# Kernel optimization log

Measured on AMD Instinct MI355X. Metric: run time of the kernel, lower is better.

Reference implementation:

```python
import jax, jax.numpy as jnp
import numpy as np

N, M, D = 1024, 32, 512
EPS = 1e-6


def setup_inputs() -> dict:
    key = jax.random.key(0)
    k1, = jax.random.split(key, 1)
    dvecs = jax.random.normal(k1, (N, M, D), dtype=jnp.float32)
    w = jnp.float32(10.0)
    b = jnp.float32(-5.0)
    return {"dvecs": dvecs, "w": w, "b": b}


def reference(dvecs, w, b):
    # dvecs: (N, M, D)
    n, m, d = dvecs.shape
    centroids = dvecs.mean(axis=1)                     # (N, D) full centroids
    # leave-one-out centroid for the reference utterance's own speaker
    c_loo = (dvecs.sum(axis=1, keepdims=True) - dvecs) / (m - 1)   # (N, M, D)

    e_norm = jnp.linalg.norm(dvecs, axis=-1)           # (N, M)
    c_norm = jnp.linalg.norm(centroids, axis=-1)       # (N,)
    c_loo_norm = jnp.linalg.norm(c_loo, axis=-1)       # (N, M)

    # cosine sim against all full centroids: (N, M, N)
    cos = jnp.einsum('jmd,kd->jmk', dvecs, centroids) / (
        e_norm[:, :, None] * c_norm[None, None, :])
    # replace the own-speaker entry with leave-one-out cosine
    loo_cos = jnp.einsum('jmd,jmd->jm', dvecs, c_loo) / (e_norm * c_loo_norm)
    jidx = jnp.arange(n)
    midx = jnp.arange(m)
    cos = cos.at[jidx[:, None], midx[None, :], jidx[:, None]].set(loo_cos)

    # torch.clamp(x, 1e-6) clamps the minimum only
    cos = jnp.maximum(cos, EPS) * w + b

    # softmax embed loss: L[j,i] = -log_softmax(cos[j,i,:])[j]
    logp = jax.nn.log_softmax(cos, axis=-1)
    L = -logp[jidx[:, None], midx[None, :], jidx[:, None]]
    return L.sum()
```

## Files before the change

kernel.cpp:

```cpp
#include <hip/hip_runtime.h>
#include <hip/hip_bf16.h>

#define NSPK 1024
#define MU 32
#define DIM 512
#define DIMP (DIM + 8)
#define NROW (NSPK * MU)
#define EPS 1e-6f

typedef __attribute__((ext_vector_type(4))) float f32x4;
typedef __attribute__((ext_vector_type(2))) long i64x2;

#define GLOAD_LDS16(g, l)                                          \
  __builtin_amdgcn_global_load_lds(                                \
      (const __attribute__((address_space(1))) void*)(g),          \
      (__attribute__((address_space(3))) void*)(l), 16, 0, 0)

__global__ __launch_bounds__(256) void k_prep(
    const float* __restrict__ dvecs,
    char* __restrict__ Af8,
    char* __restrict__ Bf8,
    float* __restrict__ loo)
{
  const int j = blockIdx.x, t = threadIdx.x;
  __shared__ float sD[MU * DIMP];
  __shared__ float4 sHalf[2][128];
  __shared__ float sS[DIM];
  __shared__ float sred[4];
  __shared__ float sS2v;
  __shared__ float sInv[MU];

  const float* base = dvecs + (size_t)j * (MU * DIM);

  const int h = t >> 7, c4 = t & 127;
  {
    const float* bp = base + h * 16 * DIM + c4 * 4;
    float4 cs = make_float4(0.f, 0.f, 0.f, 0.f);
#pragma unroll
    for (int m = 0; m < 16; ++m) {
      float4 v = *(const float4*)(bp + m * DIM);
      *(float4*)&sD[(h * 16 + m) * DIMP + c4 * 4] = v;
      cs.x += v.x; cs.y += v.y; cs.z += v.z; cs.w += v.w;
    }
    sHalf[h][c4] = cs;
  }
  __syncthreads();
  if (t < 128) {
    float4 a = sHalf[0][t], b2 = sHalf[1][t];
    float4 s;
    s.x = a.x + b2.x; s.y = a.y + b2.y; s.z = a.z + b2.z; s.w = a.w + b2.w;
    *(float4*)&sS[t * 4] = s;
  }
  __syncthreads();

  float p = sS[t] * sS[t] + sS[t + 256] * sS[t + 256];
  for (int off = 32; off; off >>= 1) p += __shfl_down(p, off);
  if ((t & 63) == 0) sred[t >> 6] = p;
  __syncthreads();
  if (t == 0) sS2v = sred[0] + sred[1] + sred[2] + sred[3];
  __syncthreads();
  const float S2 = sS2v;

  const int g = t >> 3, l = t & 7;
  float dotS = 0.f, e2 = 0.f;
  for (int i = 0; i < DIM / 8; ++i) {
    int d = i * 8 + l;
    float ev = sD[g * DIMP + d];
    dotS += ev * sS[d];
    e2 += ev * ev;
  }
  for (int off = 4; off; off >>= 1) {
    dotS += __shfl_down(dotS, off);
    e2 += __shfl_down(e2, off);
  }
  if (l == 0) {
    float numer = dotS - e2;
    float d2 = fmaxf(S2 - 2.f * dotS + e2, 1e-30f);
    loo[j * MU + g] = numer / (sqrtf(e2) * sqrtf(d2));
    sInv[g] = 1.f / sqrtf(e2);
  }
  __syncthreads();

  for (int i = 0; i < 8; ++i) {
    int idx = i * 256 + t;
    int m = idx >> 6;
    int c = idx & 63;
    int kt = c >> 2, lk = c & 3;
    float inv = sInv[m];
    const float* src = &sD[m * DIMP + c * 8];
    int b0 = 0, b1 = 0;
    b0 = __builtin_amdgcn_cvt_pk_fp8_f32(src[0] * inv, src[1] * inv, b0, false);
    b0 = __builtin_amdgcn_cvt_pk_fp8_f32(src[2] * inv, src[3] * inv, b0, true);
    b1 = __builtin_amdgcn_cvt_pk_fp8_f32(src[4] * inv, src[5] * inv, b1, false);
    b1 = __builtin_amdgcn_cvt_pk_fp8_f32(src[6] * inv, src[7] * inv, b1, true);
    size_t byte = ((size_t)(j >> 2) << 16) + ((size_t)kt << 12) +
                  ((size_t)(j & 3) << 10) + (lk * 16 + (m & 15)) * 16 +
                  (((m >> 4) & 1) << 3);
    *(int2*)(Af8 + byte) = make_int2(b0, b1);
  }

  if (t < 64) {
    int c = t;
    int kt = c >> 2, lk = c & 3;
    float invc = 1.f / sqrtf(S2);
    const float* src = &sS[c * 8];
    int b0 = 0, b1 = 0;
    b0 = __builtin_amdgcn_cvt_pk_fp8_f32(src[0] * invc, src[1] * invc, b0, false);
    b0 = __builtin_amdgcn_cvt_pk_fp8_f32(src[2] * invc, src[3] * invc, b0, true);
    b1 = __builtin_amdgcn_cvt_pk_fp8_f32(src[4] * invc, src[5] * invc, b1, false);
    b1 = __builtin_amdgcn_cvt_pk_fp8_f32(src[6] * invc, src[7] * invc, b1, true);
    size_t byte = ((size_t)(j >> 7) << 16) + ((size_t)kt << 12) +
                  ((size_t)((j >> 5) & 3) << 10) + (lk * 16 + (j & 15)) * 16 +
                  (((j >> 4) & 1) << 3);
    *(int2*)(Bf8 + byte) = make_int2(b0, b1);
  }
}

__global__ __launch_bounds__(256, 1) void k_gemm(
    const char* __restrict__ Af8,
    const char* __restrict__ Bf8,
    const float* __restrict__ wp,
    float* __restrict__ part,
    float* __restrict__ diag)
{
  __shared__ char ldsA[6 * 4096];
  __shared__ char ldsB[6 * 4096];
  __shared__ float sPart[128][2];

  const int t = threadIdx.x;
  const int w = t >> 6, lane = t & 63;
  const int lr = lane & 15, lk = lane >> 4;
  const int wm = w >> 1, wn = w & 1;
  const int bid = blockIdx.x;
  const int xcd = bid & 7, ii = bid >> 3;
  const int rb = xcd * 32 + (ii >> 3);
  const int cb = ii & 7;

  f32x4 acc[4][4];
#pragma unroll
  for (int a = 0; a < 4; ++a)
#pragma unroll
    for (int b = 0; b < 4; ++b) acc[a][b] = (f32x4)0.f;

  const char* gA = Af8 + ((size_t)rb << 16) + t * 16;
  const char* gB = Bf8 + ((size_t)cb << 16) + t * 16;
  char* dA = &ldsA[t * 16];
  char* dB = &ldsB[t * 16];

#define STAGE(kt, bi)                                          \
  {                                                            \
    GLOAD_LDS16(gA + ((size_t)(kt) << 12), dA + ((bi) << 12)); \
    GLOAD_LDS16(gB + ((size_t)(kt) << 12), dB + ((bi) << 12)); \
  }

  i64x2 aP[2][2], bP[2][2];
  const char* lA0 = &ldsA[(wm * 2) * 1024 + lane * 16];
  const char* lB0 = &ldsB[(wn * 2) * 1024 + lane * 16];

#define DSREAD(set, bi)                                      \
  {                                                          \
    aP[set][0] = *(const i64x2*)(lA0 + ((bi) << 12));        \
    aP[set][1] = *(const i64x2*)(lA0 + ((bi) << 12) + 1024); \
    bP[set][0] = *(const i64x2*)(lB0 + ((bi) << 12));        \
    bP[set][1] = *(const i64x2*)(lB0 + ((bi) << 12) + 1024); \
  }

#define MFMA_SET(s)                                                      \
  {                                                                      \
    long av[4] = {aP[s][0].x, aP[s][0].y, aP[s][1].x, aP[s][1].y};       \
    long bv[4] = {bP[s][0].x, bP[s][0].y, bP[s][1].x, bP[s][1].y};       \
    __builtin_amdgcn_s_setprio(1);                                       \
    _Pragma("unroll")                                                    \
    for (int mf = 0; mf < 4; ++mf)                                       \
      _Pragma("unroll")                                                  \
      for (int nf = 0; nf < 4; ++nf)                                     \
        acc[mf][nf] = __builtin_amdgcn_mfma_f32_16x16x32_fp8_fp8(        \
            av[mf], bv[nf], acc[mf][nf], 0, 0, 0);                       \
    __builtin_amdgcn_s_setprio(0);                                       \
  }

  STAGE(0, 0);
  STAGE(1, 1);
  STAGE(2, 2);
  STAGE(3, 3);

#pragma unroll
  for (int i = 0; i < 8; ++i) {
    if (i < 7) {
      asm volatile("s_waitcnt vmcnt(4)" ::: "memory");
    } else {
      asm volatile("s_waitcnt vmcnt(0)" ::: "memory");
    }
    __builtin_amdgcn_s_barrier();
    __builtin_amdgcn_sched_barrier(0);

    if (i <= 5) {
      STAGE(2 * i + 4, (2 * i + 4) % 6);
      STAGE(2 * i + 5, (2 * i + 5) % 6);
    }

    DSREAD(0, (2 * i) % 6);
    __builtin_amdgcn_sched_barrier(0);
    DSREAD(1, (2 * i + 1) % 6);

    asm volatile("s_waitcnt lgkmcnt(4)" ::: "memory");
    __builtin_amdgcn_sched_barrier(0);
    MFMA_SET(0);
    asm volatile("s_waitcnt lgkmcnt(0)" ::: "memory");
    __builtin_amdgcn_sched_barrier(0);
    MFMA_SET(1);
  }
#undef STAGE
#undef DSREAD
#undef MFMA_SET

  const float W = *wp;

  if (cb == (rb >> 5)) {
#pragma unroll
    for (int sp = 0; sp < 4; ++sp) {
      const int c = rb * 4 + sp;
      if (wm == (sp >> 1) && wn == ((c >> 6) & 1)) {
        const int nfo = (c >> 4) & 3;
#pragma unroll
        for (int mh = 0; mh < 2; ++mh) {
          f32x4 dsel = acc[(sp & 1) * 2 + mh][0];
#pragma unroll
          for (int nf = 1; nf < 4; ++nf)
            if (nf == nfo) dsel = acc[(sp & 1) * 2 + mh][nf];
          if (lr == (c & 15)) {
#pragma unroll
            for (int i = 0; i < 4; ++i)
              diag[c * 32 + mh * 16 + lk * 4 + i] = dsel[i];
          }
        }
      }
    }
  }

#pragma unroll
  for (int mf = 0; mf < 4; ++mf)
#pragma unroll
    for (int i = 0; i < 4; ++i) {
      float s = 0.f;
#pragma unroll
      for (int nf = 0; nf < 4; ++nf)
        s += __expf((fmaxf(acc[mf][nf][i], EPS) - 1.f) * W);
      s += __shfl_xor(s, 1);
      s += __shfl_xor(s, 2);
      s += __shfl_xor(s, 4);
      s += __shfl_xor(s, 8);
      if (lr == 0) sPart[wm * 64 + mf * 16 + lk * 4 + i][wn] = s;
    }
  __syncthreads();
  if (t < 128)
    part[(size_t)cb * NROW + rb * 128 + t] = sPart[t][0] + sPart[t][1];
}

__global__ __launch_bounds__(256) void k_final1(
    const float* __restrict__ part, const float* __restrict__ loo,
    const float* __restrict__ diag, const float* __restrict__ wp,
    float* __restrict__ p2)
{
  const int t = threadIdx.x;
  const int r = blockIdx.x * 256 + t;
  const float W = *wp;
  float s = 0.f;
#pragma unroll
  for (int c = 0; c < 8; ++c) s += part[(size_t)c * NROW + r];
  const float lt = (fmaxf(loo[r], EPS) - 1.f) * W;
  const float dt = (fmaxf(diag[r], EPS) - 1.f) * W;
  s += __expf(lt) - __expf(dt);
  float v = logf(s) - lt;
  __shared__ float red[4];
  for (int off = 32; off; off >>= 1) v += __shfl_down(v, off);
  if ((t & 63) == 0) red[t >> 6] = v;
  __syncthreads();
  if (t == 0) p2[blockIdx.x] = red[0] + red[1] + red[2] + red[3];
}

__global__ __launch_bounds__(128) void k_final2(
    const float* __restrict__ p2, float* __restrict__ out)
{
  const int t = threadIdx.x;
  float v = p2[t];
  for (int off = 32; off; off >>= 1) v += __shfl_down(v, off);
  __shared__ float red[2];
  if ((t & 63) == 0) red[t >> 6] = v;
  __syncthreads();
  if (t == 0) out[0] = red[0] + red[1];
}

extern "C" void kernel_launch(void* const* d_in, const int* in_sizes, int n_in,
                              void* d_out, int out_size, void* d_ws, size_t ws_size,
                              hipStream_t stream) {
  const float* dvecs = (const float*)d_in[0];
  const float* wptr  = (const float*)d_in[1];
  float* out = (float*)d_out;

  char* ws = (char*)d_ws;
  char* Af8 = ws;            ws += (size_t)NROW * DIM;
  char* Bf8 = ws;            ws += (size_t)NSPK * DIM;
  float* loo  = (float*)ws;  ws += (size_t)NROW * sizeof(float);
  float* diag = (float*)ws;  ws += (size_t)NROW * sizeof(float);
  float* part = (float*)ws;  ws += (size_t)8 * NROW * sizeof(float);
  float* p2   = (float*)ws;

  k_prep<<<NSPK, 256, 0, stream>>>(dvecs, Af8, Bf8, loo);
  k_gemm<<<2048, 256, 0, stream>>>(Af8, Bf8, wptr, part, diag);
  k_final1<<<NROW / 256, 256, 0, stream>>>(part, loo, diag, wptr, p2);
  k_final2<<<1, 128, 0, stream>>>(p2, out);
}
```

Baseline: 61.84 us.

## Switch FP8 GEMM to scaled 16x16x128 MFMA with repacked operand layout

Replaces the 16x16x32 FP8 MFMA with the gfx950 scaled 16x16x128 f8f6f4 MFMA using unit scales, so each instruction covers four times the K depth. The prep kernel now packs A and B into a new layout of 16-byte chunks, 32 bytes per lane per fragment, to match the new operand format. The GEMM pipeline changes from a 6-buffer 4KB staging ring to double-buffered 16KB K-tiles with four iterations, and it waits on vmcnt(0) every iteration. This cuts MFMA issue count, but the simpler pipeline exposes more load latency.

```diff
diff --git a/kernel.cpp b/kernel.cpp
--- a/kernel.cpp
+++ b/kernel.cpp
@@ -9,12 +9,14 @@
 #define EPS 1e-6f
 
 typedef __attribute__((ext_vector_type(4))) float f32x4;
-typedef __attribute__((ext_vector_type(2))) long i64x2;
+typedef __attribute__((ext_vector_type(8))) int i32x8;
 
 #define GLOAD_LDS16(g, l)                                          \
   __builtin_amdgcn_global_load_lds(                                \
       (const __attribute__((address_space(1))) void*)(g),          \
       (__attribute__((address_space(3))) void*)(l), 16, 0, 0)
+
+#define UNIT_SCALE 0x7F7F7F7F
 
 __global__ __launch_bounds__(256) void k_prep(
     const float* __restrict__ dvecs,
@@ -81,38 +83,48 @@
   }
   __syncthreads();
 
-  for (int i = 0; i < 8; ++i) {
+  for (int i = 0; i < 4; ++i) {
     int idx = i * 256 + t;
-    int m = idx >> 6;
-    int c = idx & 63;
-    int kt = c >> 2, lk = c & 3;
+    int m = idx >> 5;
+    int c = idx & 31;
+    int kt = c >> 3, kslot = (c >> 1) & 3, half = c & 1;
     float inv = sInv[m];
-    const float* src = &sD[m * DIMP + c * 8];
-    int b0 = 0, b1 = 0;
+    const float* src = &sD[m * DIMP + kt * 128 + kslot * 32 + half * 16];
+    int b0 = 0, b1 = 0, b2 = 0, b3 = 0;
     b0 = __builtin_amdgcn_cvt_pk_fp8_f32(src[0] * inv, src[1] * inv, b0, false);
     b0 = __builtin_amdgcn_cvt_pk_fp8_f32(src[2] * inv, src[3] * inv, b0, true);
     b1 = __builtin_amdgcn_cvt_pk_fp8_f32(src[4] * inv, src[5] * inv, b1, false);
     b1 = __builtin_amdgcn_cvt_pk_fp8_f32(src[6] * inv, src[7] * inv, b1, true);
-    size_t byte = ((size_t)(j >> 2) << 16) + ((size_t)kt << 12) +
-                  ((size_t)(j & 3) << 10) + (lk * 16 + (m & 15)) * 16 +
-                  (((m >> 4) & 1) << 3);
-    *(int2*)(Af8 + byte) = make_int2(b0, b1);
-  }
-
-  if (t < 64) {
+    b2 = __builtin_amdgcn_cvt_pk_fp8_f32(src[8] * inv, src[9] * inv, b2, false);
+    b2 = __builtin_amdgcn_cvt_pk_fp8_f32(src[10] * inv, src[11] * inv, b2, true);
+    b3 = __builtin_amdgcn_cvt_pk_fp8_f32(src[12] * inv, src[13] * inv, b3, false);
+    b3 = __builtin_amdgcn_cvt_pk_fp8_f32(src[14] * inv, src[15] * inv, b3, true);
+    int rp = (j & 3) * 2 + (m >> 4);
+    int lane2 = kslot * 16 + (m & 15);
+    size_t byte = (((size_t)(j >> 2) * 4 + kt) << 14) + rp * 2048 +
+                  lane2 * 32 + half * 16;
+    *(int4*)(Af8 + byte) = make_int4(b0, b1, b2, b3);
+  }
+
+  if (t < 32) {
     int c = t;
-    int kt = c >> 2, lk = c & 3;
+    int kt = c >> 3, kslot = (c >> 1) & 3, half = c & 1;
     float invc = 1.f / sqrtf(S2);
-    const float* src = &sS[c * 8];
-    int b0 = 0, b1 = 0;
+    const float* src = &sS[kt * 128 + kslot * 32 + half * 16];
+    int b0 = 0, b1 = 0, b2 = 0, b3 = 0;
     b0 = __builtin_amdgcn_cvt_pk_fp8_f32(src[0] * invc, src[1] * invc, b0, false);
     b0 = __builtin_amdgcn_cvt_pk_fp8_f32(src[2] * invc, src[3] * invc, b0, true);
     b1 = __builtin_amdgcn_cvt_pk_fp8_f32(src[4] * invc, src[5] * invc, b1, false);
     b1 = __builtin_amdgcn_cvt_pk_fp8_f32(src[6] * invc, src[7] * invc, b1, true);
-    size_t byte = ((size_t)(j >> 7) << 16) + ((size_t)kt << 12) +
-                  ((size_t)((j >> 5) & 3) << 10) + (lk * 16 + (j & 15)) * 16 +
-                  (((j >> 4) & 1) << 3);
-    *(int2*)(Bf8 + byte) = make_int2(b0, b1);
+    b2 = __builtin_amdgcn_cvt_pk_fp8_f32(src[8] * invc, src[9] * invc, b2, false);
+    b2 = __builtin_amdgcn_cvt_pk_fp8_f32(src[10] * invc, src[11] * invc, b2, true);
+    b3 = __builtin_amdgcn_cvt_pk_fp8_f32(src[12] * invc, src[13] * invc, b3, false);
+    b3 = __builtin_amdgcn_cvt_pk_fp8_f32(src[14] * invc, src[15] * invc, b3, true);
+    int rp = (j >> 4) & 7;
+    int lane2 = kslot * 16 + (j & 15);
+    size_t byte = (((size_t)(j >> 7) * 4 + kt) << 14) + rp * 2048 +
+                  lane2 * 32 + half * 16;
+    *(int4*)(Bf8 + byte) = make_int4(b0, b1, b2, b3);
   }
 }
 
@@ -123,8 +135,8 @@
     float* __restrict__ part,
     float* __restrict__ diag)
 {
-  __shared__ char ldsA[6 * 4096];
-  __shared__ char ldsB[6 * 4096];
+  __shared__ char ldsA[2 * 16384];
+  __shared__ char ldsB[2 * 16384];
   __shared__ float sPart[128][2];
 
   const int t = threadIdx.x;
@@ -147,72 +159,62 @@
   char* dA = &ldsA[t * 16];
   char* dB = &ldsB[t * 16];
 
-#define STAGE(kt, bi)                                          \
-  {                                                            \
-    GLOAD_LDS16(gA + ((size_t)(kt) << 12), dA + ((bi) << 12)); \
-    GLOAD_LDS16(gB + ((size_t)(kt) << 12), dB + ((bi) << 12)); \
-  }
-
-  i64x2 aP[2][2], bP[2][2];
-  const char* lA0 = &ldsA[(wm * 2) * 1024 + lane * 16];
-  const char* lB0 = &ldsB[(wn * 2) * 1024 + lane * 16];
-
-#define DSREAD(set, bi)                                      \
-  {                                                          \
-    aP[set][0] = *(const i64x2*)(lA0 + ((bi) << 12));        \
-    aP[set][1] = *(const i64x2*)(lA0 + ((bi) << 12) + 1024); \
-    bP[set][0] = *(const i64x2*)(lB0 + ((bi) << 12));        \
-    bP[set][1] = *(const i64x2*)(lB0 + ((bi) << 12) + 1024); \
-  }
-
-#define MFMA_SET(s)                                                      \
-  {                                                                      \
-    long av[4] = {aP[s][0].x, aP[s][0].y, aP[s][1].x, aP[s][1].y};       \
-    long bv[4] = {bP[s][0].x, bP[s][0].y, bP[s][1].x, bP[s][1].y};       \
-    __builtin_amdgcn_s_setprio(1);                                       \
-    _Pragma("unroll")                                                    \
-    for (int mf = 0; mf < 4; ++mf)                                       \
-      _Pragma("unroll")                                                  \
-      for (int nf = 0; nf < 4; ++nf)                                     \
-        acc[mf][nf] = __builtin_amdgcn_mfma_f32_16x16x32_fp8_fp8(        \
-            av[mf], bv[nf], acc[mf][nf], 0, 0, 0);                       \
-    __builtin_amdgcn_s_setprio(0);                                       \
-  }
+#define STAGE(kt, bi)                                                        \
+  {                                                                          \
+    _Pragma("unroll")                                                        \
+    for (int q = 0; q < 4; ++q) {                                            \
+      GLOAD_LDS16(gA + ((size_t)(kt) << 14) + q * 4096,                      \
+                  dA + ((bi) << 14) + q * 4096);                             \
+      GLOAD_LDS16(gB + ((size_t)(kt) << 14) + q * 4096,                      \
+                  dB + ((bi) << 14) + q * 4096);                             \
+    }                                                                        \
+  }
+
+  const char* lA0 = &ldsA[(wm * 4) * 2048 + lane * 32];
+  const char* lB0 = &ldsB[(wn * 4) * 2048 + lane * 32];
 
   STAGE(0, 0);
-  STAGE(1, 1);
-  STAGE(2, 2);
-  STAGE(3, 3);
-
-#pragma unroll
-  for (int i = 0; i < 8; ++i) {
-    if (i < 7) {
-      asm volatile("s_waitcnt vmcnt(4)" ::: "memory");
-    } else {
-      asm volatile("s_waitcnt vmcnt(0)" ::: "memory");
-    }
+
+#pragma unroll
+  for (int kt = 0; kt < 4; ++kt) {
+    asm volatile("s_waitcnt vmcnt(0)" ::: "memory");
     __builtin_amdgcn_s_barrier();
     __builtin_amdgcn_sched_barrier(0);
 
-    if (i <= 5) {
-      STAGE(2 * i + 4, (2 * i + 4) % 6);
-      STAGE(2 * i + 5, (2 * i + 5) % 6);
-    }
-
-    DSREAD(0, (2 * i) % 6);
-    __builtin_amdgcn_sched_barrier(0);
-    DSREAD(1, (2 * i + 1) % 6);
-
-    asm volatile("s_waitcnt lgkmcnt(4)" ::: "memory");
-    __builtin_amdgcn_sched_barrier(0);
-    MFMA_SET(0);
+    if (kt < 3) STAGE(kt + 1, (kt + 1) & 1);
+
+    i32x8 a8[4], b8[4];
+#pragma unroll
+    for (int f = 0; f < 4; ++f) {
+      int4 lo = *(const int4*)(lA0 + ((kt & 1) << 14) + f * 2048);
+      int4 hi = *(const int4*)(lA0 + ((kt & 1) << 14) + f * 2048 + 16);
+      a8[f][0] = lo.x; a8[f][1] = lo.y; a8[f][2] = lo.z; a8[f][3] = lo.w;
+      a8[f][4] = hi.x; a8[f][5] = hi.y; a8[f][6] = hi.z; a8[f][7] = hi.w;
+    }
+#pragma unroll
+    for (int f = 0; f < 4; ++f) {
+      int4 lo = *(const int4*)(lB0 + ((kt & 1) << 14) + f * 2048);
+      int4 hi = *(const int4*)(lB0 + ((kt & 1) << 14) + f * 2048 + 16);
+      b8[f][0] = lo.x; b8[f][1] = lo.y; b8[f][2] = lo.z; b8[f][3] = lo.w;
+      b8[f][4] = hi.x; b8[f][5] = hi.y; b8[f][6] = hi.z; b8[f][7] = hi.w;
+    }
+
     asm volatile("s_waitcnt lgkmcnt(0)" ::: "memory");
     __builtin_amdgcn_sched_barrier(0);
-    MFMA_SET(1);
+
+    __builtin_amdgcn_s_setprio(1);
+#pragma unroll
+    for (int mf = 0; mf < 4; ++mf)
+#pragma unroll
+      for (int nf = 0; nf < 4; ++nf)
+        acc[mf][nf] = __builtin_amdgcn_mfma_scale_f32_16x16x128_f8f6f4(
+            a8[mf], b8[nf], acc[mf][nf],
+            0, 0,
+            0, UNIT_SCALE,
+            0, UNIT_SCALE);
+    __builtin_amdgcn_s_setprio(0);
   }
 #undef STAGE
-#undef DSREAD
-#undef MFMA_SET
 
   const float W = *wp;
 
```

Measured after the change: 59.93 us. -3.1%, faster.
